# Kernel optimization log

Measured on AMD Instinct MI355X. Metric: run time of the kernel, lower is better.

The kernel has to match this reference:

```python
import jax, jax.numpy as jnp
import numpy as np

NUM_HEADS = 12


def setup_inputs() -> dict:
    key = jax.random.key(0)
    ks = jax.random.split(key, 9)
    R, C, B, E = 128, 256, 1, 768
    s = 1.0 / np.sqrt(E)
    return {
        "x": jax.random.normal(ks[0], (R, C, B, E), jnp.float32),
        "wq": jax.random.normal(ks[1], (E, E), jnp.float32) * s,
        "bq": jax.random.normal(ks[2], (E,), jnp.float32) * 0.02,
        "wk": jax.random.normal(ks[3], (E, E), jnp.float32) * s,
        "bk": jax.random.normal(ks[4], (E,), jnp.float32) * 0.02,
        "wv": jax.random.normal(ks[5], (E, E), jnp.float32) * s,
        "bv": jax.random.normal(ks[6], (E,), jnp.float32) * 0.02,
        "wo": jax.random.normal(ks[7], (E, E), jnp.float32) * s,
        "bo": jax.random.normal(ks[8], (E,), jnp.float32) * 0.02,
    }


def reference(x, wq, bq, wk, bk, wv, bv, wo, bo):
    R, C, B, E = x.shape
    H = NUM_HEADS
    D = E // H
    # scaling = head_dim^-0.5 / sqrt(num_rows)  (tied row attention)
    scaling = (D ** -0.5) / jnp.sqrt(jnp.asarray(R, x.dtype))
    q = (x @ wq + bq).reshape(R, C, B, H, D) * scaling
    k = (x @ wk + bk).reshape(R, C, B, H, D)
    v = (x @ wv + bv).reshape(R, C, B, H, D)
    # tied attention: contract QK^T over rows as well as head_dim
    attn_weights = jnp.einsum('ribhd,rjbhd->hbij', q, k)
    attn_probs = jax.nn.softmax(attn_weights, axis=-1)
    # same probs reused for every row
    context = jnp.einsum('hbij,rjbhd->ribhd', attn_probs, v)
    context = context.reshape(R, C, B, E)
    output = context @ wo + bo
    return (output, attn_probs)
```

## Files before the change

### kernel.cpp

```cpp
#include <hip/hip_runtime.h>
#include <hip/hip_bf16.h>
#include <stdint.h>

typedef __attribute__((ext_vector_type(4))) float f32x4;
typedef __attribute__((ext_vector_type(8))) short bf16x8;

__device__ __forceinline__ unsigned short f2bf(float f) {
  union { float f; unsigned u; } v; v.f = f;
  unsigned r = v.u + 0x7fffu + ((v.u >> 16) & 1u);
  return (unsigned short)(r >> 16);
}

#define GLL16(g, l)                                                   \
  __builtin_amdgcn_global_load_lds(                                   \
      (__attribute__((address_space(1))) void*)(g),                   \
      (__attribute__((address_space(3))) void*)(l), 16, 0, 0)

__global__ __launch_bounds__(256) void k_conv_x(const float* __restrict__ x,
                                                unsigned short* __restrict__ xb) {
  int i = blockIdx.x * 256 + threadIdx.x;
  float4 v = ((const float4*)x)[i];
  ushort4 o;
  o.x = f2bf(v.x); o.y = f2bf(v.y); o.z = f2bf(v.z); o.w = f2bf(v.w);
  ((ushort4*)xb)[i] = o;
}

__global__ __launch_bounds__(256) void k_conv_wT(const float* __restrict__ wq,
                                                 const float* __restrict__ wk,
                                                 const float* __restrict__ wv,
                                                 const float* __restrict__ wo,
                                                 unsigned short* __restrict__ WT) {
  __shared__ unsigned short tile[32][33];
  int t = blockIdx.z;
  const float* w = (t == 0) ? wq : (t == 1) ? wk : (t == 2) ? wv : wo;
  int k0 = blockIdx.x * 32, n0 = blockIdx.y * 32;
  int tx = threadIdx.x, ty = threadIdx.y;
#pragma unroll
  for (int s = 0; s < 32; s += 8)
    tile[tx][ty + s] = f2bf(w[(size_t)(k0 + ty + s) * 768 + n0 + tx]);
  __syncthreads();
#pragma unroll
  for (int s = 0; s < 32; s += 8)
    WT[(size_t)t * 589824 + (size_t)(n0 + ty + s) * 768 + k0 + tx] = tile[ty + s][tx];
}

__global__ __launch_bounds__(256) void k_gemm_qkv(const unsigned short* __restrict__ Xb,
                                                  const unsigned short* __restrict__ WT,
                                                  const float* __restrict__ bq,
                                                  const float* __restrict__ bk_,
                                                  const float* __restrict__ bv,
                                                  unsigned short* __restrict__ Q,
                                                  unsigned short* __restrict__ K,
                                                  unsigned short* __restrict__ V,
                                                  float qscale) {
  __shared__ __align__(16) unsigned short As[128 * 32];
  __shared__ __align__(16) unsigned short Bs[128 * 32];
  const int tid = threadIdx.x, lane = tid & 63, w = tid >> 6;
  const int bid = blockIdx.x;
  const int nt = bid % 18, mt = bid / 18;
  const int m0 = mt * 128;
  const int ng = nt * 128;
  const int t = ng / 768, n0 = ng % 768;
  const unsigned short* Wt = WT + (size_t)t * 589824;
  const float* bias = (t == 0) ? bq : (t == 1) ? bk_ : bv;
  unsigned short* Out = (t == 0) ? Q : (t == 1) ? K : V;
  const float scale = (t == 0) ? qscale : 1.0f;

  const int wm = w >> 1, wn = w & 1;
  const int rl4 = lane >> 2, cb4 = (lane & 3) * 16;
  const int fr = lane & 15, kb = (lane >> 4) * 16;

  f32x4 acc[4][4];
#pragma unroll
  for (int a = 0; a < 4; ++a)
#pragma unroll
    for (int b = 0; b < 4; ++b) acc[a][b] = (f32x4){0.f, 0.f, 0.f, 0.f};

  for (int k0 = 0; k0 < 768; k0 += 32) {
    __syncthreads();
#pragma unroll
    for (int c = 0; c < 2; ++c) {
      int row = w * 32 + c * 16 + rl4;
      GLL16((const char*)Xb + (size_t)(m0 + row) * 1536 + k0 * 2 + cb4,
            (char*)As + w * 2048 + c * 1024);
      GLL16((const char*)Wt + (size_t)(n0 + row) * 1536 + k0 * 2 + cb4,
            (char*)Bs + w * 2048 + c * 1024);
    }
    __syncthreads();
    bf16x8 af[4], bfr[4];
#pragma unroll
    for (int fm = 0; fm < 4; ++fm)
      af[fm] = *(const bf16x8*)((const char*)As + (wm * 64 + fm * 16 + fr) * 64 + kb);
#pragma unroll
    for (int fn = 0; fn < 4; ++fn)
      bfr[fn] = *(const bf16x8*)((const char*)Bs + (wn * 64 + fn * 16 + fr) * 64 + kb);
#pragma unroll
    for (int fm = 0; fm < 4; ++fm)
#pragma unroll
      for (int fn = 0; fn < 4; ++fn)
        acc[fm][fn] = __builtin_amdgcn_mfma_f32_16x16x32_bf16(af[fm], bfr[fn],
                                                              acc[fm][fn], 0, 0, 0);
  }

  const int rowb = (lane >> 4) * 4;
#pragma unroll
  for (int fm = 0; fm < 4; ++fm)
#pragma unroll
    for (int fn = 0; fn < 4; ++fn) {
      int col = n0 + wn * 64 + fn * 16 + fr;
      float b = bias[col];
#pragma unroll
      for (int rg = 0; rg < 4; ++rg) {
        int rowg = m0 + wm * 64 + fm * 16 + rowb + rg;
        Out[(size_t)rowg * 768 + col] = f2bf((acc[fm][fn][rg] + b) * scale);
      }
    }
}

__global__ __launch_bounds__(256) void k_attn(const unsigned short* __restrict__ Q,
                                              const unsigned short* __restrict__ Kb,
                                              float* __restrict__ logits) {
  __shared__ __align__(16) unsigned short As[128 * 64];
  __shared__ __align__(16) unsigned short Bs[128 * 64];
  const int tid = threadIdx.x, lane = tid & 63, w = tid >> 6;
  const int bid = blockIdx.x;
  const int tile = bid & 3;
  const int h = (bid >> 2) % 12;
  const int rs = bid / 48;
  const int i0 = (tile >> 1) * 128, j0 = (tile & 1) * 128;
  const int wm = w >> 1, wn = w & 1;
  const int rl8 = lane >> 3, cb8 = (lane & 7) * 16;
  const int fr = lane & 15, kb = (lane >> 4) * 16;

  f32x4 acc[4][4];
#pragma unroll
  for (int a = 0; a < 4; ++a)
#pragma unroll
    for (int b = 0; b < 4; ++b) acc[a][b] = (f32x4){0.f, 0.f, 0.f, 0.f};

  for (int rr = 0; rr < 16; ++rr) {
    int r = rs * 16 + rr;
    __syncthreads();
#pragma unroll
    for (int c = 0; c < 4; ++c) {
      int row = w * 32 + c * 8 + rl8;
      GLL16((const char*)Q + (size_t)(r * 256 + i0 + row) * 1536 + h * 128 + cb8,
            (char*)As + w * 4096 + c * 1024);
      GLL16((const char*)Kb + (size_t)(r * 256 + j0 + row) * 1536 + h * 128 + cb8,
            (char*)Bs + w * 4096 + c * 1024);
    }
    __syncthreads();
#pragma unroll
    for (int kk = 0; kk < 2; ++kk) {
      bf16x8 af[4], bfr[4];
#pragma unroll
      for (int fm = 0; fm < 4; ++fm)
        af[fm] = *(const bf16x8*)((const char*)As + (wm * 64 + fm * 16 + fr) * 128 + kk * 64 + kb);
#pragma unroll
      for (int fn = 0; fn < 4; ++fn)
        bfr[fn] = *(const bf16x8*)((const char*)Bs + (wn * 64 + fn * 16 + fr) * 128 + kk * 64 + kb);
#pragma unroll
      for (int fm = 0; fm < 4; ++fm)
#pragma unroll
        for (int fn = 0; fn < 4; ++fn)
          acc[fm][fn] = __builtin_amdgcn_mfma_f32_16x16x32_bf16(af[fm], bfr[fn],
                                                                acc[fm][fn], 0, 0, 0);
    }
  }

  float* lg = logits + (size_t)h * 65536;
  const int rowb = (lane >> 4) * 4;
#pragma unroll
  for (int fm = 0; fm < 4; ++fm)
#pragma unroll
    for (int fn = 0; fn < 4; ++fn) {
      int jj = j0 + wn * 64 + fn * 16 + fr;
#pragma unroll
      for (int rg = 0; rg < 4; ++rg) {
        int ii = i0 + wm * 64 + fm * 16 + rowb + rg;
        atomicAdd(&lg[ii * 256 + jj], acc[fm][fn][rg]);
      }
    }
}

__global__ __launch_bounds__(256) void k_softmax(const float* __restrict__ lg,
                                                 float* __restrict__ pout,
                                                 unsigned short* __restrict__ pbf) {
  const int row = blockIdx.x;
  const int j = threadIdx.x;
  const int lane = j & 63, wv = j >> 6;
  float v = lg[(size_t)row * 256 + j];
  float m = v;
#pragma unroll
  for (int o = 32; o; o >>= 1) m = fmaxf(m, __shfl_xor(m, o, 64));
  __shared__ float sm[4], ss[4];
  if (lane == 0) sm[wv] = m;
  __syncthreads();
  m = fmaxf(fmaxf(sm[0], sm[1]), fmaxf(sm[2], sm[3]));
  float e = __expf(v - m);
  float s = e;
#pragma unroll
  for (int o = 32; o; o >>= 1) s += __shfl_xor(s, o, 64);
  if (lane == 0) ss[wv] = s;
  __syncthreads();
  s = ss[0] + ss[1] + ss[2] + ss[3];
  float p = e / s;
  pout[(size_t)row * 256 + j] = p;
  pbf[(size_t)row * 256 + j] = f2bf(p);
}

__global__ __launch_bounds__(256) void k_pv(const unsigned short* __restrict__ P,
                                            const unsigned short* __restrict__ V,
                                            unsigned short* __restrict__ Cb) {
  __shared__ __align__(16) unsigned short Ps[256 * 32];
  __shared__ __align__(16) unsigned short Vs[32 * 64];
  const int tid = threadIdx.x, lane = tid & 63, w = tid >> 6;
  const int bid = blockIdx.x;
  const int h = bid % 12, r = bid / 12;
  const int fr = lane & 15, kb = (lane >> 4) * 16;
  const int rl4 = lane >> 2, cb4 = (lane & 3) * 16;
  const int rl8 = lane >> 3, cb8 = (lane & 7) * 16;

  f32x4 acc[4][4];
#pragma unroll
  for (int a = 0; a < 4; ++a)
#pragma unroll
    for (int b = 0; b < 4; ++b) acc[a][b] = (f32x4){0.f, 0.f, 0.f, 0.f};

  const char* Ph = (const char*)P + (size_t)h * 131072;
  for (int j0 = 0; j0 < 256; j0 += 32) {
    __syncthreads();
#pragma unroll
    for (int c = 0; c < 4; ++c) {
      int row = w * 64 + c * 16 + rl4;
      GLL16(Ph + (size_t)row * 512 + j0 * 2 + cb4, (char*)Ps + w * 4096 + c * 1024);
    }
    {
      int row = w * 8 + rl8;
      GLL16((const char*)V + (size_t)(r * 256 + j0 + row) * 1536 + h * 128 + cb8,
            (char*)Vs + w * 1024);
    }
    __syncthreads();
    bf16x8 af[4];
#pragma unroll
    for (int fm = 0; fm < 4; ++fm)
      af[fm] = *(const bf16x8*)((const char*)Ps + (w * 64 + fm * 16 + fr) * 64 + kb);
#pragma unroll
    for (int fn = 0; fn < 4; ++fn) {
      bf16x8 bvv;
#pragma unroll
      for (int e = 0; e < 8; ++e)
        bvv[e] = (short)Vs[(8 * (lane >> 4) + e) * 64 + fn * 16 + fr];
#pragma unroll
      for (int fm = 0; fm < 4; ++fm)
        acc[fm][fn] = __builtin_amdgcn_mfma_f32_16x16x32_bf16(af[fm], bvv,
                                                              acc[fm][fn], 0, 0, 0);
    }
  }

  const int rowb = (lane >> 4) * 4;
#pragma unroll
  for (int fm = 0; fm < 4; ++fm)
#pragma unroll
    for (int fn = 0; fn < 4; ++fn) {
      int col = h * 64 + fn * 16 + fr;
#pragma unroll
      for (int rg = 0; rg < 4; ++rg) {
        int m = r * 256 + w * 64 + fm * 16 + rowb + rg;
        Cb[(size_t)m * 768 + col] = f2bf(acc[fm][fn][rg]);
      }
    }
}

__global__ __launch_bounds__(256) void k_gemm_out(const unsigned short* __restrict__ Cb,
                                                  const unsigned short* __restrict__ WTo,
                                                  const float* __restrict__ bo,
                                                  float* __restrict__ Outp) {
  __shared__ __align__(16) unsigned short As[128 * 32];
  __shared__ __align__(16) unsigned short Bs[128 * 32];
  const int tid = threadIdx.x, lane = tid & 63, w = tid >> 6;
  const int bid = blockIdx.x;
  const int nt = bid % 6, mt = bid / 6;
  const int m0 = mt * 128, n0 = nt * 128;
  const int wm = w >> 1, wn = w & 1;
  const int rl4 = lane >> 2, cb4 = (lane & 3) * 16;
  const int fr = lane & 15, kb = (lane >> 4) * 16;

  f32x4 acc[4][4];
#pragma unroll
  for (int a = 0; a < 4; ++a)
#pragma unroll
    for (int b = 0; b < 4; ++b) acc[a][b] = (f32x4){0.f, 0.f, 0.f, 0.f};

  for (int k0 = 0; k0 < 768; k0 += 32) {
    __syncthreads();
#pragma unroll
    for (int c = 0; c < 2; ++c) {
      int row = w * 32 + c * 16 + rl4;
      GLL16((const char*)Cb + (size_t)(m0 + row) * 1536 + k0 * 2 + cb4,
            (char*)As + w * 2048 + c * 1024);
      GLL16((const char*)WTo + (size_t)(n0 + row) * 1536 + k0 * 2 + cb4,
            (char*)Bs + w * 2048 + c * 1024);
    }
    __syncthreads();
    bf16x8 af[4], bfr[4];
#pragma unroll
    for (int fm = 0; fm < 4; ++fm)
      af[fm] = *(const bf16x8*)((const char*)As + (wm * 64 + fm * 16 + fr) * 64 + kb);
#pragma unroll
    for (int fn = 0; fn < 4; ++fn)
      bfr[fn] = *(const bf16x8*)((const char*)Bs + (wn * 64 + fn * 16 + fr) * 64 + kb);
#pragma unroll
    for (int fm = 0; fm < 4; ++fm)
#pragma unroll
      for (int fn = 0; fn < 4; ++fn)
        acc[fm][fn] = __builtin_amdgcn_mfma_f32_16x16x32_bf16(af[fm], bfr[fn],
                                                              acc[fm][fn], 0, 0, 0);
  }

  const int rowb = (lane >> 4) * 4;
#pragma unroll
  for (int fm = 0; fm < 4; ++fm)
#pragma unroll
    for (int fn = 0; fn < 4; ++fn) {
      int col = n0 + wn * 64 + fn * 16 + fr;
      float b = bo[col];
#pragma unroll
      for (int rg = 0; rg < 4; ++rg) {
        int rowg = m0 + wm * 64 + fm * 16 + rowb + rg;
        Outp[(size_t)rowg * 768 + col] = acc[fm][fn][rg] + b;
      }
    }
}

extern "C" void kernel_launch(void* const* d_in, const int* in_sizes, int n_in,
                              void* d_out, int out_size, void* d_ws, size_t ws_size,
                              hipStream_t stream) {
  const float* x  = (const float*)d_in[0];
  const float* wq = (const float*)d_in[1];
  const float* bq = (const float*)d_in[2];
  const float* wk = (const float*)d_in[3];
  const float* bk = (const float*)d_in[4];
  const float* wv = (const float*)d_in[5];
  const float* bv = (const float*)d_in[6];
  const float* wo = (const float*)d_in[7];
  const float* bo = (const float*)d_in[8];
  float* out = (float*)d_out;

  char* wsb = (char*)d_ws;
  unsigned short* Cb = (unsigned short*)(wsb + 0);
  unsigned short* Qb = (unsigned short*)(wsb + 50331648);
  unsigned short* Kb = (unsigned short*)(wsb + 100663296);
  unsigned short* Vb = (unsigned short*)(wsb + 150994944);
  unsigned short* WT = (unsigned short*)(wsb + 201326592);
  float*          Lg = (float*)(wsb + 206045184);
  unsigned short* Pb = (unsigned short*)(wsb + 209190912);

  const float qscale = 0.011048543456039806f;

  k_conv_x<<<24576, 256, 0, stream>>>(x, Cb);
  k_conv_wT<<<dim3(24, 24, 4), dim3(32, 8), 0, stream>>>(wq, wk, wv, wo, WT);
  k_gemm_qkv<<<4608, 256, 0, stream>>>(Cb, WT, bq, bk, bv, Qb, Kb, Vb, qscale);
  hipMemsetAsync(Lg, 0, (size_t)12 * 256 * 256 * 4, stream);
  k_attn<<<384, 256, 0, stream>>>(Qb, Kb, Lg);
  k_softmax<<<3072, 256, 0, stream>>>(Lg, out + 25165824, Pb);
  k_pv<<<1536, 256, 0, stream>>>(Pb, Vb, Cb);
  k_gemm_out<<<1536, 256, 0, stream>>>(Cb, WT + (size_t)3 * 589824, bo, out);
}
```

Measured before the change: 328.8 us.

## Rewrite projection GEMMs as 256x256 tiles with 4-stage async LDS pipeline

Replaces the 128x128, 256-thread QKV and output projection GEMMs with a shared 256x256-tile, 512-thread core. The core prefetches three K-steps ahead into four LDS slots using global_load_lds, waits with explicit vmcnt counts, XOR-swizzles LDS to avoid bank conflicts, and raises wave priority around the MFMA block. Block indices are also remapped for L2 locality. The aim is to hide global-load latency and raise data reuse per tile. In exchange it uses 128KB of LDS per block, which allows one block per CU, and hand-tuned waitcnt logic that is fragile.

```diff
diff --git a/kernel.cpp b/kernel.cpp
--- a/kernel.cpp
+++ b/kernel.cpp
@@ -44,75 +44,151 @@
     WT[(size_t)t * 589824 + (size_t)(n0 + ty + s) * 768 + k0 + tx] = tile[ty + s][tx];
 }
 
-__global__ __launch_bounds__(256) void k_gemm_qkv(const unsigned short* __restrict__ Xb,
-                                                  const unsigned short* __restrict__ WT,
-                                                  const float* __restrict__ bq,
-                                                  const float* __restrict__ bk_,
-                                                  const float* __restrict__ bv,
-                                                  unsigned short* __restrict__ Q,
-                                                  unsigned short* __restrict__ K,
-                                                  unsigned short* __restrict__ V,
-                                                  float qscale) {
-  __shared__ __align__(16) unsigned short As[128 * 32];
-  __shared__ __align__(16) unsigned short Bs[128 * 32];
+__device__ __forceinline__ void gemm256_core(const char* __restrict__ Ag,
+                                             const char* __restrict__ Bg,
+                                             char* lds, int tid,
+                                             f32x4 (&acc)[8][4]) {
+  const int lane = tid & 63, w = tid >> 6;
+  const int wm = w >> 2, wn = w & 3;
+  const int fr = lane & 15, kb = (lane >> 4) * 16;
+  const bool stageB = (w >= 4);
+  const char* Sg = stageB ? Bg : Ag;
+  const int wrow0 = 64 * (w & 3);
+  const int srow = lane >> 2;
+  const int slotL = lane & 3;
+
+#pragma unroll
+  for (int t = 0; t < 3; ++t) {
+    char* dslot = lds + t * 32768 + (stageB ? 16384 : 0);
+#pragma unroll
+    for (int c = 0; c < 4; ++c) {
+      int row = wrow0 + c * 16 + srow;
+      int sG = slotL ^ ((row >> 1) & 3);
+      GLL16(Sg + (size_t)row * 1536 + t * 64 + sG * 16,
+            dslot + (wrow0 + c * 16) * 64);
+    }
+  }
+
+  for (int t = 0; t < 24; ++t) {
+    if (t < 22)       asm volatile("s_waitcnt vmcnt(8)" ::: "memory");
+    else if (t == 22) asm volatile("s_waitcnt vmcnt(4)" ::: "memory");
+    else              asm volatile("s_waitcnt vmcnt(0)" ::: "memory");
+    __builtin_amdgcn_s_barrier();
+
+    const char* slot = lds + (t & 3) * 32768;
+    bf16x8 af[8], bfr[4];
+#pragma unroll
+    for (int fm = 0; fm < 8; ++fm) {
+      int row = wm * 128 + fm * 16 + fr;
+      af[fm] = *(const bf16x8*)(slot + row * 64 + (kb ^ (((row >> 1) & 3) << 4)));
+    }
+#pragma unroll
+    for (int fn = 0; fn < 4; ++fn) {
+      int row = wn * 64 + fn * 16 + fr;
+      bfr[fn] = *(const bf16x8*)(slot + 16384 + row * 64 + (kb ^ (((row >> 1) & 3) << 4)));
+    }
+
+    if (t + 3 < 24) {
+      char* dslot = lds + ((t + 3) & 3) * 32768 + (stageB ? 16384 : 0);
+#pragma unroll
+      for (int c = 0; c < 4; ++c) {
+        int row = wrow0 + c * 16 + srow;
+        int sG = slotL ^ ((row >> 1) & 3);
+        GLL16(Sg + (size_t)row * 1536 + (t + 3) * 64 + sG * 16,
+              dslot + (wrow0 + c * 16) * 64);
+      }
+    }
+
+    __builtin_amdgcn_s_setprio(1);
+#pragma unroll
+    for (int fm = 0; fm < 8; ++fm)
+#pragma unroll
+      for (int fn = 0; fn < 4; ++fn)
+        acc[fm][fn] = __builtin_amdgcn_mfma_f32_16x16x32_bf16(af[fm], bfr[fn],
+                                                              acc[fm][fn], 0, 0, 0);
+    __builtin_amdgcn_s_setprio(0);
+  }
+}
+
+__global__ __launch_bounds__(512, 1) void k_gemm_qkv(const unsigned short* __restrict__ Xb,
+                                                     const unsigned short* __restrict__ WT,
+                                                     const float* __restrict__ bq,
+                                                     const float* __restrict__ bk_,
+                                                     const float* __restrict__ bv,
+                                                     unsigned short* __restrict__ Q,
+                                                     unsigned short* __restrict__ K,
+                                                     unsigned short* __restrict__ V,
+                                                     float qscale) {
+  __shared__ __align__(16) char lds[131072];
   const int tid = threadIdx.x, lane = tid & 63, w = tid >> 6;
   const int bid = blockIdx.x;
-  const int nt = bid % 18, mt = bid / 18;
-  const int m0 = mt * 128;
-  const int ng = nt * 128;
-  const int t = ng / 768, n0 = ng % 768;
+  const int swz = (bid & 7) * 144 + (bid >> 3);
+  const int mt = swz / 9, nt = swz % 9;
+  const int m0 = mt * 256;
+  const int t = nt / 3, n0 = (nt % 3) * 256;
+
   const unsigned short* Wt = WT + (size_t)t * 589824;
   const float* bias = (t == 0) ? bq : (t == 1) ? bk_ : bv;
   unsigned short* Out = (t == 0) ? Q : (t == 1) ? K : V;
   const float scale = (t == 0) ? qscale : 1.0f;
 
-  const int wm = w >> 1, wn = w & 1;
-  const int rl4 = lane >> 2, cb4 = (lane & 3) * 16;
-  const int fr = lane & 15, kb = (lane >> 4) * 16;
-
-  f32x4 acc[4][4];
-#pragma unroll
-  for (int a = 0; a < 4; ++a)
+  f32x4 acc[8][4];
+#pragma unroll
+  for (int a = 0; a < 8; ++a)
 #pragma unroll
     for (int b = 0; b < 4; ++b) acc[a][b] = (f32x4){0.f, 0.f, 0.f, 0.f};
 
-  for (int k0 = 0; k0 < 768; k0 += 32) {
-    __syncthreads();
-#pragma unroll
-    for (int c = 0; c < 2; ++c) {
-      int row = w * 32 + c * 16 + rl4;
-      GLL16((const char*)Xb + (size_t)(m0 + row) * 1536 + k0 * 2 + cb4,
-            (char*)As + w * 2048 + c * 1024);
-      GLL16((const char*)Wt + (size_t)(n0 + row) * 1536 + k0 * 2 + cb4,
-            (char*)Bs + w * 2048 + c * 1024);
-    }
-    __syncthreads();
-    bf16x8 af[4], bfr[4];
-#pragma unroll
-    for (int fm = 0; fm < 4; ++fm)
-      af[fm] = *(const bf16x8*)((const char*)As + (wm * 64 + fm * 16 + fr) * 64 + kb);
-#pragma unroll
-    for (int fn = 0; fn < 4; ++fn)
-      bfr[fn] = *(const bf16x8*)((const char*)Bs + (wn * 64 + fn * 16 + fr) * 64 + kb);
-#pragma unroll
-    for (int fm = 0; fm < 4; ++fm)
-#pragma unroll
-      for (int fn = 0; fn < 4; ++fn)
-        acc[fm][fn] = __builtin_amdgcn_mfma_f32_16x16x32_bf16(af[fm], bfr[fn],
-                                                              acc[fm][fn], 0, 0, 0);
-  }
-
-  const int rowb = (lane >> 4) * 4;
-#pragma unroll
-  for (int fm = 0; fm < 4; ++fm)
+  gemm256_core((const char*)Xb + (size_t)m0 * 1536,
+               (const char*)Wt + (size_t)n0 * 1536, lds, tid, acc);
+
+  const int wm = w >> 2, wn = w & 3;
+  const int fr = lane & 15, rowb = (lane >> 4) * 4;
+#pragma unroll
+  for (int fm = 0; fm < 8; ++fm)
 #pragma unroll
     for (int fn = 0; fn < 4; ++fn) {
       int col = n0 + wn * 64 + fn * 16 + fr;
       float b = bias[col];
 #pragma unroll
       for (int rg = 0; rg < 4; ++rg) {
-        int rowg = m0 + wm * 64 + fm * 16 + rowb + rg;
-        Out[(size_t)rowg * 768 + col] = f2bf((acc[fm][fn][rg] + b) * scale);
+        int row = m0 + wm * 128 + fm * 16 + rowb + rg;
+        Out[(size_t)row * 768 + col] = f2bf((acc[fm][fn][rg] + b) * scale);
+      }
+    }
+}
+
+__global__ __launch_bounds__(512, 1) void k_gemm_out(const unsigned short* __restrict__ Cb,
+                                                     const unsigned short* __restrict__ WTo,
+                                                     const float* __restrict__ bo,
+                                                     float* __restrict__ Outp) {
+  __shared__ __align__(16) char lds[131072];
+  const int tid = threadIdx.x, lane = tid & 63, w = tid >> 6;
+  const int bid = blockIdx.x;
+  const int swz = (bid & 7) * 48 + (bid >> 3);
+  const int mt = swz / 3, nt = swz % 3;
+  const int m0 = mt * 256, n0 = nt * 256;
+
+  f32x4 acc[8][4];
+#pragma unroll
+  for (int a = 0; a < 8; ++a)
+#pragma unroll
+    for (int b = 0; b < 4; ++b) acc[a][b] = (f32x4){0.f, 0.f, 0.f, 0.f};
+
+  gemm256_core((const char*)Cb + (size_t)m0 * 1536,
+               (const char*)WTo + (size_t)n0 * 1536, lds, tid, acc);
+
+  const int wm = w >> 2, wn = w & 3;
+  const int fr = lane & 15, rowb = (lane >> 4) * 4;
+#pragma unroll
+  for (int fm = 0; fm < 8; ++fm)
+#pragma unroll
+    for (int fn = 0; fn < 4; ++fn) {
+      int col = n0 + wn * 64 + fn * 16 + fr;
+      float b = bo[col];
+#pragma unroll
+      for (int rg = 0; rg < 4; ++rg) {
+        int row = m0 + wm * 128 + fm * 16 + rowb + rg;
+        Outp[(size_t)row * 768 + col] = acc[fm][fn][rg] + b;
       }
     }
 }
@@ -272,67 +348,6 @@
     }
 }
 
-__global__ __launch_bounds__(256) void k_gemm_out(const unsigned short* __restrict__ Cb,
-                                                  const unsigned short* __restrict__ WTo,
-                                                  const float* __restrict__ bo,
-                                                  float* __restrict__ Outp) {
-  __shared__ __align__(16) unsigned short As[128 * 32];
-  __shared__ __align__(16) unsigned short Bs[128 * 32];
-  const int tid = threadIdx.x, lane = tid & 63, w = tid >> 6;
-  const int bid = blockIdx.x;
-  const int nt = bid % 6, mt = bid / 6;
-  const int m0 = mt * 128, n0 = nt * 128;
-  const int wm = w >> 1, wn = w & 1;
-  const int rl4 = lane >> 2, cb4 = (lane & 3) * 16;
-  const int fr = lane & 15, kb = (lane >> 4) * 16;
-
-  f32x4 acc[4][4];
-#pragma unroll
-  for (int a = 0; a < 4; ++a)
-#pragma unroll
-    for (int b = 0; b < 4; ++b) acc[a][b] = (f32x4){0.f, 0.f, 0.f, 0.f};
-
-  for (int k0 = 0; k0 < 768; k0 += 32) {
-    __syncthreads();
-#pragma unroll
-    for (int c = 0; c < 2; ++c) {
-      int row = w * 32 + c * 16 + rl4;
-      GLL16((const char*)Cb + (size_t)(m0 + row) * 1536 + k0 * 2 + cb4,
-            (char*)As + w * 2048 + c * 1024);
-      GLL16((const char*)WTo + (size_t)(n0 + row) * 1536 + k0 * 2 + cb4,
-            (char*)Bs + w * 2048 + c * 1024);
-    }
-    __syncthreads();
-    bf16x8 af[4], bfr[4];
-#pragma unroll
-    for (int fm = 0; fm < 4; ++fm)
-      af[fm] = *(const bf16x8*)((const char*)As + (wm * 64 + fm * 16 + fr) * 64 + kb);
-#pragma unroll
-    for (int fn = 0; fn < 4; ++fn)
-      bfr[fn] = *(const bf16x8*)((const char*)Bs + (wn * 64 + fn * 16 + fr) * 64 + kb);
-#pragma unroll
-    for (int fm = 0; fm < 4; ++fm)
-#pragma unroll
-      for (int fn = 0; fn < 4; ++fn)
-        acc[fm][fn] = __builtin_amdgcn_mfma_f32_16x16x32_bf16(af[fm], bfr[fn],
-                                                              acc[fm][fn], 0, 0, 0);
-  }
-
-  const int rowb = (lane >> 4) * 4;
-#pragma unroll
-  for (int fm = 0; fm < 4; ++fm)
-#pragma unroll
-    for (int fn = 0; fn < 4; ++fn) {
-      int col = n0 + wn * 64 + fn * 16 + fr;
-      float b = bo[col];
-#pragma unroll
-      for (int rg = 0; rg < 4; ++rg) {
-        int rowg = m0 + wm * 64 + fm * 16 + rowb + rg;
-        Outp[(size_t)rowg * 768 + col] = acc[fm][fn][rg] + b;
-      }
-    }
-}
-
 extern "C" void kernel_launch(void* const* d_in, const int* in_sizes, int n_in,
                               void* d_out, int out_size, void* d_ws, size_t ws_size,
                               hipStream_t stream) {
@@ -360,10 +375,10 @@
 
   k_conv_x<<<24576, 256, 0, stream>>>(x, Cb);
   k_conv_wT<<<dim3(24, 24, 4), dim3(32, 8), 0, stream>>>(wq, wk, wv, wo, WT);
-  k_gemm_qkv<<<4608, 256, 0, stream>>>(Cb, WT, bq, bk, bv, Qb, Kb, Vb, qscale);
+  k_gemm_qkv<<<1152, 512, 0, stream>>>(Cb, WT, bq, bk, bv, Qb, Kb, Vb, qscale);
   hipMemsetAsync(Lg, 0, (size_t)12 * 256 * 256 * 4, stream);
   k_attn<<<384, 256, 0, stream>>>(Qb, Kb, Lg);
   k_softmax<<<3072, 256, 0, stream>>>(Lg, out + 25165824, Pb);
   k_pv<<<1536, 256, 0, stream>>>(Pb, Vb, Cb);
-  k_gemm_out<<<1536, 256, 0, stream>>>(Cb, WT + (size_t)3 * 589824, bo, out);
-}
+  k_gemm_out<<<384, 512, 0, stream>>>(Cb, WT + (size_t)3 * 589824, bo, out);
+}
```

Result: faster. 286.2 us (-13.0%).
